# Kernel optimization log

Measured on AMD Instinct MI355X. Metric: run time of the kernel, lower is better.

## Reference

```python
import jax, jax.numpy as jnp
import numpy as np

B, S, D, H = 16, 1024, 1024, 16
HD = D // H  # head_dim = 64
SCALE = HD ** -0.5


def setup_inputs() -> dict:
    key = jax.random.key(0)
    ks = jax.random.split(key, 9)
    init = 1.0 / np.sqrt(D)
    x = jax.random.normal(ks[0], (B, S, D), dtype=jnp.float32)
    Wq = jax.random.normal(ks[1], (D, D), dtype=jnp.float32) * init
    bq = jnp.zeros((D,), dtype=jnp.float32)
    Wk = jax.random.normal(ks[2], (D, D), dtype=jnp.float32) * init
    bk = jnp.zeros((D,), dtype=jnp.float32)
    Wv = jax.random.normal(ks[3], (D, D), dtype=jnp.float32) * init
    bv = jnp.zeros((D,), dtype=jnp.float32)
    Wo = jax.random.normal(ks[4], (D, D), dtype=jnp.float32) * init
    bo = jnp.zeros((D,), dtype=jnp.float32)
    return {"x": x, "Wq": Wq, "bq": bq, "Wk": Wk, "bk": bk,
            "Wv": Wv, "bv": bv, "Wo": Wo, "bo": bo}


def reference(x, Wq, bq, Wk, bk, Wv, bv, Wo, bo):
    # QKV projections: [B,S,D] -> [B,H,S,HD]
    def split_heads(t):
        return t.reshape(B, S, H, HD).transpose(0, 2, 1, 3)

    q = split_heads(x @ Wq + bq)
    k = split_heads(x @ Wk + bk)
    v = split_heads(x @ Wv + bv)

    # scores [B,H,S,S]; softmax in fp32 then cast back (matches torch dtype=float32)
    scores = jnp.einsum("bhqd,bhkd->bhqk", q, k) * SCALE
    attn = jax.nn.softmax(scores.astype(jnp.float32), axis=-1).astype(q.dtype)
    # dropout p=0.0 -> identity

    out = jnp.einsum("bhqk,bhkd->bhqd", attn, v)  # [B,H,S,HD]
    out = out.transpose(0, 2, 1, 3).reshape(B, S, D)
    out = out @ Wo + bo
    return out, attn
```

## Files before the change

kernel.cpp:

```cpp
#include <hip/hip_runtime.h>
#include <hip/hip_bf16.h>
#include <cstddef>

#define Bsz 16
#define Ssz 1024
#define Dsz 1024
#define Hn  16
#define HDs 64
#define SCALE_F 0.125f

typedef unsigned short ushort_t;
typedef __bf16 bf16x8 __attribute__((ext_vector_type(8)));
typedef float f32x4 __attribute__((ext_vector_type(4)));
typedef ushort_t u16x4 __attribute__((ext_vector_type(4)));

#define MFMA16(a, b, c) __builtin_amdgcn_mfma_f32_16x16x32_bf16((a), (b), (c), 0, 0, 0)

__device__ inline ushort_t bf16u(float f) {
    __bf16 h = (__bf16)f;
    return __builtin_bit_cast(ushort_t, h);
}

__device__ inline float bf16f(ushort_t u) {
    return __builtin_bit_cast(float, (unsigned)u << 16);
}

__device__ inline void gld_lds16(const void* g, void* l) {
    __builtin_amdgcn_global_load_lds(
        (const __attribute__((address_space(1))) unsigned int*)g,
        (__attribute__((address_space(3))) unsigned int*)l, 16, 0, 0);
}

__global__ __launch_bounds__(256) void cast_k(const float* __restrict__ in,
                                              ushort_t* __restrict__ o, size_t n)
{
    size_t i = ((size_t)blockIdx.x * 256 + threadIdx.x) * 8;
    if (i >= n) return;
    float4 a = *(const float4*)(in + i);
    float4 b = *(const float4*)(in + i + 4);
    union { ushort_t u[8]; uint4 v; } pk;
    pk.u[0] = bf16u(a.x); pk.u[1] = bf16u(a.y); pk.u[2] = bf16u(a.z); pk.u[3] = bf16u(a.w);
    pk.u[4] = bf16u(b.x); pk.u[5] = bf16u(b.y); pk.u[6] = bf16u(b.z); pk.u[7] = bf16u(b.w);
    *(uint4*)(o + i) = pk.v;
}

__global__ __launch_bounds__(256) void wtrans_k(
    const float* __restrict__ W0, const float* __restrict__ W1,
    const float* __restrict__ W2, const float* __restrict__ W3,
    ushort_t* __restrict__ T012, ushort_t* __restrict__ T3)
{
    __shared__ float t_[32][33];
    const int tx = threadIdx.x, ty = threadIdx.y;
    const int n0 = blockIdx.x * 32, k0 = blockIdx.y * 32;
    const int z = blockIdx.z;
    const float* W = (z == 0) ? W0 : (z == 1) ? W1 : (z == 2) ? W2 : W3;
    ushort_t* Wt = (z < 3) ? (T012 + (size_t)z * Dsz * Dsz) : T3;
    #pragma unroll
    for (int i = 0; i < 4; ++i)
        t_[ty + i * 8][tx] = W[(size_t)(k0 + ty + i * 8) * Dsz + n0 + tx];
    __syncthreads();
    #pragma unroll
    for (int i = 0; i < 4; ++i)
        Wt[(size_t)(n0 + ty + i * 8) * Dsz + k0 + tx] = bf16u(t_[tx][ty + i * 8]);
}

template <int MODE>
__global__ __launch_bounds__(256) void gemm_bt_k(
    const ushort_t* __restrict__ A, const ushort_t* __restrict__ Bt,
    const float* __restrict__ b0, const float* __restrict__ b1,
    const float* __restrict__ b2,
    void* __restrict__ o0, void* __restrict__ o1, void* __restrict__ o2,
    int M, int N, int K)
{
    __shared__ ushort_t shmem[MODE == 1 ? 128 * 132 : 128 * 64];
    ushort_t* As = shmem;
    ushort_t* Bs = shmem + 128 * 32;

    const int tid = threadIdx.x;
    const int lane = tid & 63;
    const int wv = tid >> 6;
    const int wr = wv >> 1, wc = wv & 1;
    const int bm = blockIdx.y * 128, bn = blockIdx.x * 128;

    const int srw = tid >> 2;
    const int gc = (tid & 3) ^ ((srw >> 1) & 3);
    const ushort_t* aptr0 = A + (size_t)(bm + srw) * K + gc * 8;
    const ushort_t* aptr1 = A + (size_t)(bm + 64 + srw) * K + gc * 8;
    const ushort_t* bptr0 = Bt + (size_t)(bn + srw) * K + gc * 8;
    const ushort_t* bptr1 = Bt + (size_t)(bn + 64 + srw) * K + gc * 8;
    ushort_t* lA0 = As + tid * 8;
    ushort_t* lA1 = As + 2048 + tid * 8;
    ushort_t* lB0 = Bs + tid * 8;
    ushort_t* lB1 = Bs + 2048 + tid * 8;

    const int am = lane & 15;
    const int rc = lane >> 4;
    const int aslot = rc ^ ((am >> 1) & 3);
    const int rrow_a = wr * 64 + am;
    const int rrow_b = wc * 64 + am;

    f32x4 acc[4][4] = {};

    for (int k0 = 0; k0 < K; k0 += 32) {
        if (k0) __syncthreads();
        gld_lds16(aptr0, lA0); gld_lds16(aptr1, lA1);
        gld_lds16(bptr0, lB0); gld_lds16(bptr1, lB1);
        aptr0 += 32; aptr1 += 32; bptr0 += 32; bptr1 += 32;
        __syncthreads();

        bf16x8 af[4], bfr[4];
        #pragma unroll
        for (int m = 0; m < 4; ++m)
            af[m] = *reinterpret_cast<const bf16x8*>(&As[(rrow_a + m * 16) * 32 + aslot * 8]);
        #pragma unroll
        for (int n = 0; n < 4; ++n)
            bfr[n] = *reinterpret_cast<const bf16x8*>(&Bs[(rrow_b + n * 16) * 32 + aslot * 8]);
        #pragma unroll
        for (int m = 0; m < 4; ++m)
            #pragma unroll
            for (int n = 0; n < 4; ++n)
                acc[m][n] = MFMA16(af[m], bfr[n], acc[m][n]);
    }

    const int erow = rc * 4;

    if constexpr (MODE == 0) {
        float* C = (float*)o0;
        #pragma unroll
        for (int m = 0; m < 4; ++m) {
            #pragma unroll
            for (int n = 0; n < 4; ++n) {
                const int col = bn + wc * 64 + n * 16 + am;
                const float bv = b0[col];
                #pragma unroll
                for (int r = 0; r < 4; ++r) {
                    const int row = bm + wr * 64 + m * 16 + erow + r;
                    C[(size_t)row * N + col] = acc[m][n][r] + bv;
                }
            }
        }
    } else {
        const int tsel = bn >> 10;
        const float* bias = (tsel == 0) ? b0 : (tsel == 1) ? b1 : b2;
        ushort_t* dst = (ushort_t*)((tsel == 0) ? o0 : (tsel == 1) ? o1 : o2);
        const int bnm = bn & 1023;

        if (tsel == 2) {
            #pragma unroll
            for (int m = 0; m < 4; ++m) {
                const int row0 = bm + wr * 64 + m * 16 + erow;
                const int b_ = row0 >> 10;
                const int srow0 = row0 & 1023;
                #pragma unroll
                for (int n = 0; n < 4; ++n) {
                    const int c1 = bnm + wc * 64 + n * 16 + am;
                    const int h = c1 >> 6, d = c1 & 63;
                    const float bv = bias[c1];
                    const size_t hb = ((size_t)(b_ * 16 + h)) << 16;
                    const size_t base = hb + (size_t)(d >> 4) * 16384
                                      + (srow0 >> 5) * 512
                                      + (((srow0 >> 3) & 3) * 16 + (d & 15)) * 8
                                      + (srow0 & 7);
                    u16x4 pk;
                    pk.x = bf16u(acc[m][n][0] + bv);
                    pk.y = bf16u(acc[m][n][1] + bv);
                    pk.z = bf16u(acc[m][n][2] + bv);
                    pk.w = bf16u(acc[m][n][3] + bv);
                    *(u16x4*)&dst[base] = pk;
                }
            }
        } else {
            __syncthreads();
            #pragma unroll
            for (int m = 0; m < 4; ++m) {
                const int srow = wr * 64 + m * 16 + erow;
                #pragma unroll
                for (int n = 0; n < 4; ++n) {
                    const int ccol = wc * 64 + n * 16 + am;
                    const float bv = bias[bnm + ccol];
                    u16x4 pk;
                    if (tsel == 0) {
                        pk.x = bf16u((acc[m][n][0] + bv) * SCALE_F);
                        pk.y = bf16u((acc[m][n][1] + bv) * SCALE_F);
                        pk.z = bf16u((acc[m][n][2] + bv) * SCALE_F);
                        pk.w = bf16u((acc[m][n][3] + bv) * SCALE_F);
                    } else {
                        pk.x = bf16u(acc[m][n][0] + bv);
                        pk.y = bf16u(acc[m][n][1] + bv);
                        pk.z = bf16u(acc[m][n][2] + bv);
                        pk.w = bf16u(acc[m][n][3] + bv);
                    }
                    *(u16x4*)&shmem[ccol * 132 + srow] = pk;
                }
            }
            __syncthreads();
            #pragma unroll
            for (int j = 0; j < 8; ++j) {
                const int idx = j * 256 + tid;
                const int s  = idx >> 4;
                const int c8 = idx & 15;
                union { ushort_t u[8]; uint4 v; } pk;
                #pragma unroll
                for (int e = 0; e < 8; ++e)
                    pk.u[e] = shmem[(c8 * 8 + e) * 132 + s];
                const int row = bm + s;
                const int b_ = row >> 10;
                const int srow0 = row & 1023;
                const int h = (bnm >> 6) + (c8 >> 3);
                const int d0 = (c8 & 7) * 8;
                const size_t hb = ((size_t)(b_ * 16 + h)) << 16;
                size_t gaddr;
                if (tsel == 0) {
                    gaddr = hb + (size_t)srow0 * 64 + d0;
                } else {
                    gaddr = hb + (size_t)(srow0 >> 4) * 1024
                          + (d0 >> 5) * 512
                          + (((d0 >> 3) & 3) * 16 + (srow0 & 15)) * 8;
                }
                *(uint4*)&dst[gaddr] = pk.v;
            }
        }
    }
}

__global__ __launch_bounds__(256, 4) void attn_fused_k(
    const ushort_t* __restrict__ Qh, const ushort_t* __restrict__ Kp,
    const ushort_t* __restrict__ Vp, float* __restrict__ attn,
    ushort_t* __restrict__ ctx)
{
    __shared__ ushort_t Pl[16 * 1024];
    __shared__ float ssum[4][16];

    const int tid = threadIdx.x;
    const int lane = tid & 63;
    const int wv = tid >> 6;
    const int am = lane & 15;
    const int ak = lane >> 4;
    const int kb = wv * 256;

    const int wg = blockIdx.x;
    const int swz = (wg & 7) * 2048 + (wg >> 3);
    const int bh = swz >> 6;
    const int q0 = (swz & 63) << 4;
    const int b = bh >> 4, h = bh & 15;
    const size_t hb = (size_t)bh << 16;

    const ushort_t* qptr = Qh + hb + (size_t)(q0 + am) * 64 + ak * 8;
    const bf16x8 qf0 = *(const bf16x8*)qptr;
    const bf16x8 qf1 = *(const bf16x8*)(qptr + 32);

    f32x4 acc[16];
    #pragma unroll
    for (int n = 0; n < 16; ++n) acc[n] = (f32x4){0.f, 0.f, 0.f, 0.f};

    const ushort_t* kt = Kp + hb + (size_t)(wv * 16) * 1024 + lane * 8;
    __builtin_amdgcn_s_setprio(1);
    #pragma unroll
    for (int n = 0; n < 16; ++n) {
        const bf16x8 kf0 = *(const bf16x8*)(kt + n * 1024);
        const bf16x8 kf1 = *(const bf16x8*)(kt + n * 1024 + 512);
        acc[n] = MFMA16(kf0, qf0, acc[n]);
        acc[n] = MFMA16(kf1, qf1, acc[n]);
    }
    __builtin_amdgcn_s_setprio(0);

    float s = 0.f;
    #pragma unroll
    for (int n = 0; n < 16; ++n)
        #pragma unroll
        for (int r = 0; r < 4; ++r) {
            const float e = __expf(fminf(acc[n][r], 60.0f));
            acc[n][r] = e;
            s += e;
        }
    s += __shfl_xor(s, 16);
    s += __shfl_xor(s, 32);
    if (ak == 0) ssum[wv][am] = s;

    char* prow = (char*)Pl + am * 2048;
    const int xr = (am & 7) << 4;
    #pragma unroll
    for (int n = 0; n < 16; ++n) {
        u16x4 pk;
        pk.x = bf16u(acc[n][0]); pk.y = bf16u(acc[n][1]);
        pk.z = bf16u(acc[n][2]); pk.w = bf16u(acc[n][3]);
        *(u16x4*)(prow + (((kb + n * 16 + ak * 4) * 2) ^ xr)) = pk;
    }
    __syncthreads();

    const ushort_t* vt = Vp + hb + (size_t)wv * 16384 + lane * 8;
    bf16x8 v0 = *(const bf16x8*)(vt);
    bf16x8 v1 = *(const bf16x8*)(vt + 512);
    bf16x8 v2 = *(const bf16x8*)(vt + 1024);
    bf16x8 v3 = *(const bf16x8*)(vt + 1536);

    {
        float* aout = attn + ((size_t)bh * Ssz + q0) * Ssz;
        #pragma unroll
        for (int j = 0; j < 16; ++j) {
            const float invj = 1.0f / (ssum[0][j] + ssum[1][j] +
                                       ssum[2][j] + ssum[3][j]);
            const u16x4 pw = *(const u16x4*)((char*)Pl + j * 2048 +
                                             ((tid * 8) ^ ((j & 7) << 4)));
            f32x4 v;
            v[0] = bf16f(pw.x) * invj; v[1] = bf16f(pw.y) * invj;
            v[2] = bf16f(pw.z) * invj; v[3] = bf16f(pw.w) * invj;
            __builtin_nontemporal_store(v, (f32x4*)(aout + (size_t)j * Ssz + tid * 4));
        }
    }

    f32x4 po = {0.f, 0.f, 0.f, 0.f};
    __builtin_amdgcn_s_setprio(1);
    #pragma unroll
    for (int w = 0; w < 32; w += 4) {
        const bf16x8 p0 = *(const bf16x8*)(prow + (((w + 0) * 64 + ak * 16) ^ xr));
        const bf16x8 p1 = *(const bf16x8*)(prow + (((w + 1) * 64 + ak * 16) ^ xr));
        const bf16x8 p2 = *(const bf16x8*)(prow + (((w + 2) * 64 + ak * 16) ^ xr));
        const bf16x8 p3 = *(const bf16x8*)(prow + (((w + 3) * 64 + ak * 16) ^ xr));
        po = MFMA16(p0, v0, po);
        if (w + 4 < 32) v0 = *(const bf16x8*)(vt + (w + 4) * 512);
        po = MFMA16(p1, v1, po);
        if (w + 5 < 32) v1 = *(const bf16x8*)(vt + (w + 5) * 512);
        po = MFMA16(p2, v2, po);
        if (w + 6 < 32) v2 = *(const bf16x8*)(vt + (w + 6) * 512);
        po = MFMA16(p3, v3, po);
        if (w + 7 < 32) v3 = *(const bf16x8*)(vt + (w + 7) * 512);
    }
    __builtin_amdgcn_s_setprio(0);

    #pragma unroll
    for (int r = 0; r < 4; ++r) {
        const int q = ak * 4 + r;
        const float invq = 1.0f / (ssum[0][q] + ssum[1][q] +
                                   ssum[2][q] + ssum[3][q]);
        ctx[((size_t)b * Ssz + q0 + q) * Dsz + h * HDs + wv * 16 + am] =
            bf16u(po[r] * invq);
    }
}

extern "C" void kernel_launch(void* const* d_in, const int* in_sizes, int n_in,
                              void* d_out, int out_size, void* d_ws, size_t ws_size,
                              hipStream_t stream)
{
    const float* x  = (const float*)d_in[0];
    const float* Wq = (const float*)d_in[1];
    const float* bq = (const float*)d_in[2];
    const float* Wk = (const float*)d_in[3];
    const float* bk = (const float*)d_in[4];
    const float* Wv = (const float*)d_in[5];
    const float* bv = (const float*)d_in[6];
    const float* Wo = (const float*)d_in[7];
    const float* bo = (const float*)d_in[8];

    const size_t BSD = (size_t)Bsz * Ssz * Dsz;
    const size_t WSZ = (size_t)Dsz * Dsz;

    float* outp = (float*)d_out;
    float* attn = outp + BSD;

    ushort_t* xbf  = (ushort_t*)d_ws;
    ushort_t* Qh   = xbf + BSD;
    ushort_t* Kp   = Qh + BSD;
    ushort_t* Vp   = Kp + BSD;
    ushort_t* ctxb = Vp + BSD;
    ushort_t* Wqkv = ctxb + BSD;
    ushort_t* Wot  = Wqkv + 3 * WSZ;

    const int M = Bsz * Ssz;

    cast_k<<<dim3((unsigned)(BSD / 2048)), 256, 0, stream>>>(x, xbf, BSD);

    wtrans_k<<<dim3(32, 32, 4), dim3(32, 8), 0, stream>>>(
        Wq, Wk, Wv, Wo, Wqkv, Wot);

    gemm_bt_k<1><<<dim3(24, 128), 256, 0, stream>>>(
        xbf, Wqkv, bq, bk, bv, Qh, Kp, Vp, M, 3072, Dsz);

    attn_fused_k<<<dim3(16384), 256, 0, stream>>>(Qh, Kp, Vp, attn, ctxb);

    gemm_bt_k<0><<<dim3(8, 128), 256, 0, stream>>>(
        ctxb, Wot, bo, nullptr, nullptr, outp, nullptr, nullptr, M, Dsz, Dsz);
}
```

Before: 472.3 us.

## Process two 16-query tiles per attention block to reuse K/V loads

Each attention workgroup now handles 32 query rows instead of 16, sharing each K and V fragment load across two MFMA accumulator sets. The grid is halved and shared memory for probabilities and row sums is doubled. The aim is to cut redundant K/V global traffic per query. In exchange it doubles accumulator registers and LDS per block and lowers the occupancy target from 4 to 2 blocks per CU, which may reduce latency hiding for the large attention-matrix store.

```diff
diff --git a/kernel.cpp b/kernel.cpp
--- a/kernel.cpp
+++ b/kernel.cpp
@@ -215,7 +215,7 @@
                 } else {
                     gaddr = hb + (size_t)(srow0 >> 4) * 1024
                           + (d0 >> 5) * 512
-                          + (((d0 >> 3) & 3) * 16 + (srow0 & 15)) * 8;
+                          + (((d0 >> 3) & 3) * 16 + (srow0 & 15) ) * 8;
                 }
                 *(uint4*)&dst[gaddr] = pk.v;
             }
@@ -223,35 +223,39 @@
     }
 }
 
-__global__ __launch_bounds__(256, 4) void attn_fused_k(
+__global__ __launch_bounds__(256, 2) void attn_fused_k(
     const ushort_t* __restrict__ Qh, const ushort_t* __restrict__ Kp,
     const ushort_t* __restrict__ Vp, float* __restrict__ attn,
     ushort_t* __restrict__ ctx)
 {
-    __shared__ ushort_t Pl[16 * 1024];
-    __shared__ float ssum[4][16];
+    __shared__ ushort_t Pl[32 * 1024];
+    __shared__ float ssum[4][32];
 
     const int tid = threadIdx.x;
     const int lane = tid & 63;
     const int wv = tid >> 6;
     const int am = lane & 15;
     const int ak = lane >> 4;
-    const int kb = wv * 256;
 
     const int wg = blockIdx.x;
-    const int swz = (wg & 7) * 2048 + (wg >> 3);
-    const int bh = swz >> 6;
-    const int q0 = (swz & 63) << 4;
+    const int swz = (wg & 7) * 1024 + (wg >> 3);
+    const int bh = swz >> 5;
+    const int q0 = (swz & 31) << 5;
     const int b = bh >> 4, h = bh & 15;
     const size_t hb = (size_t)bh << 16;
 
-    const ushort_t* qptr = Qh + hb + (size_t)(q0 + am) * 64 + ak * 8;
-    const bf16x8 qf0 = *(const bf16x8*)qptr;
-    const bf16x8 qf1 = *(const bf16x8*)(qptr + 32);
-
-    f32x4 acc[16];
-    #pragma unroll
-    for (int n = 0; n < 16; ++n) acc[n] = (f32x4){0.f, 0.f, 0.f, 0.f};
+    const ushort_t* qptrA = Qh + hb + (size_t)(q0 + am) * 64 + ak * 8;
+    const bf16x8 qfA0 = *(const bf16x8*)qptrA;
+    const bf16x8 qfA1 = *(const bf16x8*)(qptrA + 32);
+    const bf16x8 qfB0 = *(const bf16x8*)(qptrA + 16 * 64);
+    const bf16x8 qfB1 = *(const bf16x8*)(qptrA + 16 * 64 + 32);
+
+    f32x4 accA[16], accB[16];
+    #pragma unroll
+    for (int n = 0; n < 16; ++n) {
+        accA[n] = (f32x4){0.f, 0.f, 0.f, 0.f};
+        accB[n] = (f32x4){0.f, 0.f, 0.f, 0.f};
+    }
 
     const ushort_t* kt = Kp + hb + (size_t)(wv * 16) * 1024 + lane * 8;
     __builtin_amdgcn_s_setprio(1);
@@ -259,32 +263,41 @@
     for (int n = 0; n < 16; ++n) {
         const bf16x8 kf0 = *(const bf16x8*)(kt + n * 1024);
         const bf16x8 kf1 = *(const bf16x8*)(kt + n * 1024 + 512);
-        acc[n] = MFMA16(kf0, qf0, acc[n]);
-        acc[n] = MFMA16(kf1, qf1, acc[n]);
+        accA[n] = MFMA16(kf0, qfA0, accA[n]);
+        accA[n] = MFMA16(kf1, qfA1, accA[n]);
+        accB[n] = MFMA16(kf0, qfB0, accB[n]);
+        accB[n] = MFMA16(kf1, qfB1, accB[n]);
     }
     __builtin_amdgcn_s_setprio(0);
 
-    float s = 0.f;
+    float sA = 0.f, sB = 0.f;
     #pragma unroll
     for (int n = 0; n < 16; ++n)
         #pragma unroll
         for (int r = 0; r < 4; ++r) {
-            const float e = __expf(fminf(acc[n][r], 60.0f));
-            acc[n][r] = e;
-            s += e;
+            const float eA = __expf(fminf(accA[n][r], 60.0f));
+            accA[n][r] = eA; sA += eA;
+            const float eB = __expf(fminf(accB[n][r], 60.0f));
+            accB[n][r] = eB; sB += eB;
         }
-    s += __shfl_xor(s, 16);
-    s += __shfl_xor(s, 32);
-    if (ak == 0) ssum[wv][am] = s;
-
-    char* prow = (char*)Pl + am * 2048;
+    sA += __shfl_xor(sA, 16); sA += __shfl_xor(sA, 32);
+    sB += __shfl_xor(sB, 16); sB += __shfl_xor(sB, 32);
+    if (ak == 0) { ssum[wv][am] = sA; ssum[wv][16 + am] = sB; }
+
+    const int kb = wv * 256;
+    char* prowA = (char*)Pl + am * 2048;
+    char* prowB = (char*)Pl + (16 + am) * 2048;
     const int xr = (am & 7) << 4;
     #pragma unroll
     for (int n = 0; n < 16; ++n) {
-        u16x4 pk;
-        pk.x = bf16u(acc[n][0]); pk.y = bf16u(acc[n][1]);
-        pk.z = bf16u(acc[n][2]); pk.w = bf16u(acc[n][3]);
-        *(u16x4*)(prow + (((kb + n * 16 + ak * 4) * 2) ^ xr)) = pk;
+        const int off = ((kb + n * 16 + ak * 4) * 2) ^ xr;
+        u16x4 pa, pb;
+        pa.x = bf16u(accA[n][0]); pa.y = bf16u(accA[n][1]);
+        pa.z = bf16u(accA[n][2]); pa.w = bf16u(accA[n][3]);
+        pb.x = bf16u(accB[n][0]); pb.y = bf16u(accB[n][1]);
+        pb.z = bf16u(accB[n][2]); pb.w = bf16u(accB[n][3]);
+        *(u16x4*)(prowA + off) = pa;
+        *(u16x4*)(prowB + off) = pb;
     }
     __syncthreads();
 
@@ -297,7 +310,7 @@
     {
         float* aout = attn + ((size_t)bh * Ssz + q0) * Ssz;
         #pragma unroll
-        for (int j = 0; j < 16; ++j) {
+        for (int j = 0; j < 32; ++j) {
             const float invj = 1.0f / (ssum[0][j] + ssum[1][j] +
                                        ssum[2][j] + ssum[3][j]);
             const u16x4 pw = *(const u16x4*)((char*)Pl + j * 2048 +
@@ -309,32 +322,42 @@
         }
     }
 
-    f32x4 po = {0.f, 0.f, 0.f, 0.f};
+    f32x4 poA = {0.f, 0.f, 0.f, 0.f};
+    f32x4 poB = {0.f, 0.f, 0.f, 0.f};
     __builtin_amdgcn_s_setprio(1);
     #pragma unroll
     for (int w = 0; w < 32; w += 4) {
-        const bf16x8 p0 = *(const bf16x8*)(prow + (((w + 0) * 64 + ak * 16) ^ xr));
-        const bf16x8 p1 = *(const bf16x8*)(prow + (((w + 1) * 64 + ak * 16) ^ xr));
-        const bf16x8 p2 = *(const bf16x8*)(prow + (((w + 2) * 64 + ak * 16) ^ xr));
-        const bf16x8 p3 = *(const bf16x8*)(prow + (((w + 3) * 64 + ak * 16) ^ xr));
-        po = MFMA16(p0, v0, po);
+        const int o0 = ((w + 0) * 64 + ak * 16) ^ xr;
+        const int o1 = ((w + 1) * 64 + ak * 16) ^ xr;
+        const int o2 = ((w + 2) * 64 + ak * 16) ^ xr;
+        const int o3 = ((w + 3) * 64 + ak * 16) ^ xr;
+        poA = MFMA16(*(const bf16x8*)(prowA + o0), v0, poA);
+        poB = MFMA16(*(const bf16x8*)(prowB + o0), v0, poB);
         if (w + 4 < 32) v0 = *(const bf16x8*)(vt + (w + 4) * 512);
-        po = MFMA16(p1, v1, po);
+        poA = MFMA16(*(const bf16x8*)(prowA + o1), v1, poA);
+        poB = MFMA16(*(const bf16x8*)(prowB + o1), v1, poB);
         if (w + 5 < 32) v1 = *(const bf16x8*)(vt + (w + 5) * 512);
-        po = MFMA16(p2, v2, po);
+        poA = MFMA16(*(const bf16x8*)(prowA + o2), v2, poA);
+        poB = MFMA16(*(const bf16x8*)(prowB + o2), v2, poB);
         if (w + 6 < 32) v2 = *(const bf16x8*)(vt + (w + 6) * 512);
-        po = MFMA16(p3, v3, po);
+        poA = MFMA16(*(const bf16x8*)(prowA + o3), v3, poA);
+        poB = MFMA16(*(const bf16x8*)(prowB + o3), v3, poB);
         if (w + 7 < 32) v3 = *(const bf16x8*)(vt + (w + 7) * 512);
     }
     __builtin_amdgcn_s_setprio(0);
 
     #pragma unroll
     for (int r = 0; r < 4; ++r) {
-        const int q = ak * 4 + r;
-        const float invq = 1.0f / (ssum[0][q] + ssum[1][q] +
-                                   ssum[2][q] + ssum[3][q]);
-        ctx[((size_t)b * Ssz + q0 + q) * Dsz + h * HDs + wv * 16 + am] =
-            bf16u(po[r] * invq);
+        const int qA = ak * 4 + r;
+        const float invA = 1.0f / (ssum[0][qA] + ssum[1][qA] +
+                                   ssum[2][qA] + ssum[3][qA]);
+        ctx[((size_t)b * Ssz + q0 + qA) * Dsz + h * HDs + wv * 16 + am] =
+            bf16u(poA[r] * invA);
+        const int qB = 16 + qA;
+        const float invB = 1.0f / (ssum[0][qB] + ssum[1][qB] +
+                                   ssum[2][qB] + ssum[3][qB]);
+        ctx[((size_t)b * Ssz + q0 + qB) * Dsz + h * HDs + wv * 16 + am] =
+            bf16u(poB[r] * invB);
     }
 }
 
@@ -376,7 +399,7 @@
     gemm_bt_k<1><<<dim3(24, 128), 256, 0, stream>>>(
         xbf, Wqkv, bq, bk, bv, Qh, Kp, Vp, M, 3072, Dsz);
 
-    attn_fused_k<<<dim3(16384), 256, 0, stream>>>(Qh, Kp, Vp, attn, ctxb);
+    attn_fused_k<<<dim3(8192), 256, 0, stream>>>(Qh, Kp, Vp, attn, ctxb);
 
     gemm_bt_k<0><<<dim3(8, 128), 256, 0, stream>>>(
         ctxb, Wot, bo, nullptr, nullptr, outp, nullptr, nullptr, M, Dsz, Dsz);
```

After: 467.5 us. About the same (-1.0%).
